# Kernel optimization log

Measured on AMD Instinct MI355X. Metric: run time of the kernel, lower is better.

The kernel has to match this reference:

```python
import jax, jax.numpy as jnp
import numpy as np

L = 16            # number of levels
F = 2             # features per level
T = 1 << 17       # hashmap size per level (power of 2)
N_TREES = 8       # forest blocks
N = 2_000_000     # query points
RES = np.array([16, 22, 30, 41, 55, 75, 102, 139, 188, 256, 348, 472, 642, 872, 1184, 1608], dtype=np.int64)
# 8 trilinear corner offsets [8,3]
OFFS = np.stack(np.meshgrid([0, 1], [0, 1], [0, 1], indexing='ij'), axis=-1).reshape(8, 3).astype(np.int32)
PRIMES = (np.uint32(1), np.uint32(2654435761), np.uint32(805459861))


def _hash(coords):
    # coords: [N,8,3] int32 grid corner coords -> [N,8] table index (NGP spatial hash)
    c = coords.astype(jnp.uint32)
    h = (c[..., 0] * PRIMES[0]) ^ (c[..., 1] * PRIMES[1]) ^ (c[..., 2] * PRIMES[2])
    return (h & jnp.uint32(T - 1)).astype(jnp.int32)


def setup_inputs() -> dict:
    key = jax.random.key(0)
    k1, k2, k3 = jax.random.split(key, 3)
    block_x = jax.random.uniform(k1, (N, 3), minval=-1.0, maxval=1.0, dtype=jnp.float32)
    bound = 1e-4
    params = jax.random.uniform(k2, (N_TREES, L, T, F), minval=-bound, maxval=bound, dtype=jnp.float32)
    block_inds = jax.random.randint(k3, (N,), 0, N_TREES)
    return {"block_x": block_x, "params": params, "block_inds": block_inds}


def reference(block_x, params, block_inds):
    # block_x in [-1,1]^3 -> [0,1]^3 (matches `block_x / 2.0 + 0.5` in forward)
    x01 = block_x * 0.5 + 0.5
    offs = jnp.asarray(OFFS)                    # [8,3]
    offs_b = jnp.asarray(OFFS, dtype=bool)      # [8,3]
    outs = []
    for l in range(L):
        R = int(RES[l])
        pos = x01 * (R - 1)                     # [N,3]
        p0 = jnp.floor(pos)
        w = pos - p0                            # trilinear fracs [N,3]
        p0i = p0.astype(jnp.int32)
        corners = jnp.clip(p0i[:, None, :] + offs[None], 0, R - 1)   # [N,8,3]
        idx = _hash(corners)                                          # [N,8]
        feats = params[block_inds[:, None], l, idx, :]                # [N,8,F] per-tree gather
        wc = jnp.prod(jnp.where(offs_b[None], w[:, None, :], 1.0 - w[:, None, :]), axis=-1)  # [N,8]
        outs.append(jnp.einsum('nc,ncf->nf', wc, feats))              # [N,F]
    return jnp.concatenate(outs, axis=-1)        # [N, L*F]
```

## Files before the change

kernel.cpp:

```cpp
#include <hip/hip_runtime.h>

#define NLEVELS 16
#define TSIZE 131072
#define TMASK (TSIZE - 1)
#define NBUCK 32768

typedef float f32x4 __attribute__((ext_vector_type(4)));

__device__ __constant__ float RM1_TAB[16] = {
    15.f, 21.f, 29.f, 40.f, 54.f, 74.f, 101.f, 138.f,
    187.f, 255.f, 347.f, 471.f, 641.f, 871.f, 1183.f, 1607.f
};

__device__ __forceinline__ unsigned spread4(unsigned v) {
    v = (v | (v << 4)) & 0x0C3u;
    v = (v | (v << 2)) & 0x249u;
    return v;
}

__device__ __forceinline__ unsigned bucket_key(float x, float y, float z, unsigned tree) {
    const int cx = min(max((int)((x * 0.5f + 0.5f) * 16.f), 0), 15);
    const int cy = min(max((int)((y * 0.5f + 0.5f) * 16.f), 0), 15);
    const int cz = min(max((int)((z * 0.5f + 0.5f) * 16.f), 0), 15);
    const unsigned m = spread4((unsigned)cx) | (spread4((unsigned)cy) << 1)
                     | (spread4((unsigned)cz) << 2);
    return (tree << 12) | m;
}


__global__ __launch_bounds__(256) void k_hist(const float* __restrict__ xs,
                                              const int* __restrict__ inds, int N,
                                              unsigned* __restrict__ hist) {
    const int i = blockIdx.x * 256 + threadIdx.x;
    if (i >= N) return;
    const unsigned key = bucket_key(xs[3 * i], xs[3 * i + 1], xs[3 * i + 2],
                                    (unsigned)(inds[i] & 7));
    atomicAdd(&hist[key], 1u);
}

__global__ __launch_bounds__(1024) void k_scan(const unsigned* __restrict__ hist,
                                               unsigned* __restrict__ cursor) {
    __shared__ unsigned sums[1024];
    const int t = threadIdx.x;
    const int per = NBUCK / 1024;
    unsigned s = 0;
    #pragma unroll
    for (int j = 0; j < per; ++j) s += hist[t * per + j];
    sums[t] = s;
    __syncthreads();
    for (int off = 1; off < 1024; off <<= 1) {
        const unsigned add = (t >= off) ? sums[t - off] : 0u;
        __syncthreads();
        sums[t] += add;
        __syncthreads();
    }
    unsigned run = (t == 0) ? 0u : sums[t - 1];
    #pragma unroll
    for (int j = 0; j < per; ++j) {
        cursor[t * per + j] = run;
        run += hist[t * per + j];
    }
}

__global__ __launch_bounds__(256) void k_scatter(const float* __restrict__ xs,
                                                 const int* __restrict__ inds, int N,
                                                 unsigned* __restrict__ cursor,
                                                 float4* __restrict__ sorted) {
    const int i = blockIdx.x * 256 + threadIdx.x;
    if (i >= N) return;
    const float x = xs[3 * i], y = xs[3 * i + 1], z = xs[3 * i + 2];
    const unsigned tree = (unsigned)(inds[i] & 7);
    const unsigned key = bucket_key(x, y, z, tree);
    const unsigned pos = atomicAdd(&cursor[key], 1u);
    sorted[pos] = make_float4(x, y, z, __uint_as_float(((unsigned)i) | (tree << 24)));
}


__global__ __launch_bounds__(256) void k_main(const float4* __restrict__ sorted,
                                              const float* __restrict__ params,
                                              float4* __restrict__ ws2,
                                              float4* __restrict__ out4,
                                              int N, int nc, int direct) {
    const int b = blockIdx.x;
    const int k = b & 7;
    const int chunk = b >> 3;
    const int i = chunk * 256 + threadIdx.x;
    if (i >= N) return;

    const float4 p = sorted[i];
    const unsigned wbits = __float_as_uint(p.w);
    const int n = (int)(wbits & 0xFFFFFFu);
    const int tree = (int)(wbits >> 24);

    float acc[4];

    #pragma unroll
    for (int kk = 0; kk < 2; ++kk) {
        const int l = 2 * k + kk;
        const float rm1 = RM1_TAB[l];
        const int rmax = (int)rm1;

        const float px = (p.x * 0.5f + 0.5f) * rm1;
        const float py = (p.y * 0.5f + 0.5f) * rm1;
        const float pz = (p.z * 0.5f + 0.5f) * rm1;
        const float fx = floorf(px), fy = floorf(py), fz = floorf(pz);
        const float wx = px - fx, wy = py - fy, wz = pz - fz;
        const int ix = (int)fx, iy = (int)fy, iz = (int)fz;

        const int x0 = min(max(ix, 0), rmax), x1 = min(max(ix + 1, 0), rmax);
        const int y0 = min(max(iy, 0), rmax), y1 = min(max(iy + 1, 0), rmax);
        const int z0 = min(max(iz, 0), rmax), z1 = min(max(iz + 1, 0), rmax);

        const unsigned hx0 = (unsigned)x0;
        const unsigned hx1 = (unsigned)x1;
        const unsigned hy0 = (unsigned)y0 * 2654435761u;
        const unsigned hy1 = (unsigned)y1 * 2654435761u;
        const unsigned hz0 = (unsigned)z0 * 805459861u;
        const unsigned hz1 = (unsigned)z1 * 805459861u;

        const float2* __restrict__ tbl =
            (const float2*)(params + (size_t)(tree * NLEVELS + l) * (TSIZE * 2));

        const unsigned m00 = hy0 ^ hz0;
        const unsigned m01 = hy0 ^ hz1;
        const unsigned m10 = hy1 ^ hz0;
        const unsigned m11 = hy1 ^ hz1;
        const unsigned i000 = (hx0 ^ m00) & TMASK;
        const unsigned i001 = (hx0 ^ m01) & TMASK;
        const unsigned i010 = (hx0 ^ m10) & TMASK;
        const unsigned i011 = (hx0 ^ m11) & TMASK;

        float2 f000, f001, f010, f011, f100, f101, f110, f111;

        const bool pairOK = ((x0 & 1) == 0) && (x1 == x0 + 1);
        if (pairOK) {
            const float4* __restrict__ tbl4 = (const float4*)tbl;
            const float4 q00 = tbl4[i000 >> 1];
            const float4 q01 = tbl4[i001 >> 1];
            const float4 q10 = tbl4[i010 >> 1];
            const float4 q11 = tbl4[i011 >> 1];
            f000 = (i000 & 1) ? make_float2(q00.z, q00.w) : make_float2(q00.x, q00.y);
            f100 = (i000 & 1) ? make_float2(q00.x, q00.y) : make_float2(q00.z, q00.w);
            f001 = (i001 & 1) ? make_float2(q01.z, q01.w) : make_float2(q01.x, q01.y);
            f101 = (i001 & 1) ? make_float2(q01.x, q01.y) : make_float2(q01.z, q01.w);
            f010 = (i010 & 1) ? make_float2(q10.z, q10.w) : make_float2(q10.x, q10.y);
            f110 = (i010 & 1) ? make_float2(q10.x, q10.y) : make_float2(q10.z, q10.w);
            f011 = (i011 & 1) ? make_float2(q11.z, q11.w) : make_float2(q11.x, q11.y);
            f111 = (i011 & 1) ? make_float2(q11.x, q11.y) : make_float2(q11.z, q11.w);
        } else {
            const unsigned i100 = (hx1 ^ m00) & TMASK;
            const unsigned i101 = (hx1 ^ m01) & TMASK;
            const unsigned i110 = (hx1 ^ m10) & TMASK;
            const unsigned i111 = (hx1 ^ m11) & TMASK;
            f000 = tbl[i000]; f001 = tbl[i001];
            f010 = tbl[i010]; f011 = tbl[i011];
            f100 = tbl[i100]; f101 = tbl[i101];
            f110 = tbl[i110]; f111 = tbl[i111];
        }

        const float wx0 = 1.f - wx, wy0 = 1.f - wy, wz0 = 1.f - wz;

        const float w000 = wx0 * wy0 * wz0;
        const float w001 = wx0 * wy0 * wz;
        const float w010 = wx0 * wy  * wz0;
        const float w011 = wx0 * wy  * wz;
        const float w100 = wx  * wy0 * wz0;
        const float w101 = wx  * wy0 * wz;
        const float w110 = wx  * wy  * wz0;
        const float w111 = wx  * wy  * wz;

        float a0 = 0.f, a1 = 0.f;
        a0 = fmaf(w000, f000.x, a0); a1 = fmaf(w000, f000.y, a1);
        a0 = fmaf(w001, f001.x, a0); a1 = fmaf(w001, f001.y, a1);
        a0 = fmaf(w010, f010.x, a0); a1 = fmaf(w010, f010.y, a1);
        a0 = fmaf(w011, f011.x, a0); a1 = fmaf(w011, f011.y, a1);
        a0 = fmaf(w100, f100.x, a0); a1 = fmaf(w100, f100.y, a1);
        a0 = fmaf(w101, f101.x, a0); a1 = fmaf(w101, f101.y, a1);
        a0 = fmaf(w110, f110.x, a0); a1 = fmaf(w110, f110.y, a1);
        a0 = fmaf(w111, f111.x, a0); a1 = fmaf(w111, f111.y, a1);

        acc[2 * kk + 0] = a0;
        acc[2 * kk + 1] = a1;
    }

    const float4 v = make_float4(acc[0], acc[1], acc[2], acc[3]);
    if (direct) {
        out4[(size_t)n * 8 + k] = v;
    } else {
        const size_t stride = (size_t)nc * 256;
        __builtin_nontemporal_store(*(const f32x4*)&v,
                                    (f32x4*)&ws2[(size_t)k * stride + i]);
    }
}


__global__ __launch_bounds__(256) void k_final(const float4* __restrict__ sorted,
                                               const float4* __restrict__ ws2,
                                               float4* __restrict__ out4,
                                               int N, int nc) {
    const int i = blockIdx.x * 256 + threadIdx.x;
    if (i >= N) return;
    const unsigned wbits = __float_as_uint(sorted[i].w);
    const int n = (int)(wbits & 0xFFFFFFu);
    const size_t stride = (size_t)nc * 256;
    #pragma unroll
    for (int k = 0; k < 8; ++k) {
        f32x4 v = __builtin_nontemporal_load((const f32x4*)&ws2[(size_t)k * stride + i]);
        out4[(size_t)n * 8 + k] = *(const float4*)&v;
    }
}


__global__ __launch_bounds__(256) void lotd_fwd_fused(
    const float* __restrict__ xs, const float* __restrict__ params,
    const int* __restrict__ inds, float* __restrict__ out, int N)
{
    const int g = blockIdx.x * 256 + threadIdx.x;
    const int n = g >> 4;
    if (n >= N) return;
    const int l = g & 15;
    const float rm1 = RM1_TAB[l];
    const int rmax = (int)rm1;
    const float x = xs[3 * n], y = xs[3 * n + 1], z = xs[3 * n + 2];
    const int tree = inds[n];
    const float px = (x * 0.5f + 0.5f) * rm1;
    const float py = (y * 0.5f + 0.5f) * rm1;
    const float pz = (z * 0.5f + 0.5f) * rm1;
    const float fx = floorf(px), fy = floorf(py), fz = floorf(pz);
    const float wx = px - fx, wy = py - fy, wz = pz - fz;
    const int ix = (int)fx, iy = (int)fy, iz = (int)fz;
    const int x0 = min(max(ix, 0), rmax), x1 = min(max(ix + 1, 0), rmax);
    const int y0 = min(max(iy, 0), rmax), y1 = min(max(iy + 1, 0), rmax);
    const int z0 = min(max(iz, 0), rmax), z1 = min(max(iz + 1, 0), rmax);
    const unsigned hx0 = (unsigned)x0, hx1 = (unsigned)x1;
    const unsigned hy0 = (unsigned)y0 * 2654435761u, hy1 = (unsigned)y1 * 2654435761u;
    const unsigned hz0 = (unsigned)z0 * 805459861u,  hz1 = (unsigned)z1 * 805459861u;
    const float2* tbl = (const float2*)(params + (size_t)(tree * NLEVELS + l) * (TSIZE * 2));
    const float2 f000 = tbl[(hx0 ^ hy0 ^ hz0) & TMASK];
    const float2 f001 = tbl[(hx0 ^ hy0 ^ hz1) & TMASK];
    const float2 f010 = tbl[(hx0 ^ hy1 ^ hz0) & TMASK];
    const float2 f011 = tbl[(hx0 ^ hy1 ^ hz1) & TMASK];
    const float2 f100 = tbl[(hx1 ^ hy0 ^ hz0) & TMASK];
    const float2 f101 = tbl[(hx1 ^ hy0 ^ hz1) & TMASK];
    const float2 f110 = tbl[(hx1 ^ hy1 ^ hz0) & TMASK];
    const float2 f111 = tbl[(hx1 ^ hy1 ^ hz1) & TMASK];
    const float wx0 = 1.f - wx, wy0 = 1.f - wy, wz0 = 1.f - wz;
    float a0 = 0.f, a1 = 0.f;
    a0 = fmaf(wx0*wy0*wz0, f000.x, a0); a1 = fmaf(wx0*wy0*wz0, f000.y, a1);
    a0 = fmaf(wx0*wy0*wz , f001.x, a0); a1 = fmaf(wx0*wy0*wz , f001.y, a1);
    a0 = fmaf(wx0*wy *wz0, f010.x, a0); a1 = fmaf(wx0*wy *wz0, f010.y, a1);
    a0 = fmaf(wx0*wy *wz , f011.x, a0); a1 = fmaf(wx0*wy *wz , f011.y, a1);
    a0 = fmaf(wx *wy0*wz0, f100.x, a0); a1 = fmaf(wx *wy0*wz0, f100.y, a1);
    a0 = fmaf(wx *wy0*wz , f101.x, a0); a1 = fmaf(wx *wy0*wz , f101.y, a1);
    a0 = fmaf(wx *wy *wz0, f110.x, a0); a1 = fmaf(wx *wy *wz0, f110.y, a1);
    a0 = fmaf(wx *wy *wz , f111.x, a0); a1 = fmaf(wx *wy *wz , f111.y, a1);
    ((float2*)out)[(size_t)n * 16 + l] = make_float2(a0, a1);
}

extern "C" void kernel_launch(void* const* d_in, const int* in_sizes, int n_in,
                              void* d_out, int out_size, void* d_ws, size_t ws_size,
                              hipStream_t stream) {
    const float* xs     = (const float*)d_in[0];
    const float* params = (const float*)d_in[1];
    const int*   inds   = (const int*)d_in[2];
    float*       out    = (float*)d_out;

    const int N = in_sizes[0] / 3;
    const int nc = (N + 255) / 256;

    const size_t hist_bytes   = (size_t)NBUCK * 4;
    const size_t head_bytes   = 2 * hist_bytes;
    const size_t sorted_bytes = ((size_t)N * 16 + 255) & ~(size_t)255;
    const size_t ws2_bytes    = (size_t)nc * 256 * 8 * 16;
    const size_t need_B = head_bytes + sorted_bytes;
    const size_t need_A = need_B + ws2_bytes;

    if (ws_size < need_B) {
        const int total = N * NLEVELS;
        lotd_fwd_fused<<<(total + 255) / 256, 256, 0, stream>>>(xs, params, inds, out, N);
        return;
    }

    unsigned* hist   = (unsigned*)d_ws;
    unsigned* cursor = (unsigned*)((char*)d_ws + hist_bytes);
    float4*   sorted = (float4*)((char*)d_ws + head_bytes);
    float4*   ws2    = (float4*)((char*)d_ws + head_bytes + sorted_bytes);

    hipMemsetAsync(hist, 0, hist_bytes, stream);
    k_hist<<<nc, 256, 0, stream>>>(xs, inds, N, hist);
    k_scan<<<1, 1024, 0, stream>>>(hist, cursor);
    k_scatter<<<nc, 256, 0, stream>>>(xs, inds, N, cursor, sorted);

    const int direct = (ws_size < need_A) ? 1 : 0;
    k_main<<<nc * 8, 256, 0, stream>>>(sorted, params,
                                       direct ? nullptr : ws2,
                                       (float4*)out, N, nc, direct);
    if (!direct)
        k_final<<<nc, 256, 0, stream>>>(sorted, ws2, (float4*)out, N, nc);
}
```

Before: 949.5 us.

## Drop staging buffer, write outputs directly with banded level rotation

Removes the intermediate ws2 buffer and the k_final gather kernel, so k_main now scatters its float4 results straight to the output rows. The level pair each block handles is rotated by band index, so concurrently running blocks touch different level tables and spread the gather traffic. It also issues both levels' table loads before either FMA reduction to raise memory-level parallelism. The trade-off is uncoalesced scattered writes in place of a coalesced staging pass, in exchange for saving a full write-plus-read of the intermediate data and one launch.

```diff
diff --git a/kernel.cpp b/kernel.cpp
--- a/kernel.cpp
+++ b/kernel.cpp
@@ -76,14 +76,103 @@
 }
 
 
+__device__ __forceinline__ void level_load(const float4 p, int tree, int l,
+                                           const float* __restrict__ params,
+                                           float2 f[8],
+                                           float& wx, float& wy, float& wz) {
+    const float rm1 = RM1_TAB[l];
+    const int rmax = (int)rm1;
+
+    const float px = (p.x * 0.5f + 0.5f) * rm1;
+    const float py = (p.y * 0.5f + 0.5f) * rm1;
+    const float pz = (p.z * 0.5f + 0.5f) * rm1;
+    const float fx = floorf(px), fy = floorf(py), fz = floorf(pz);
+    wx = px - fx; wy = py - fy; wz = pz - fz;
+    const int ix = (int)fx, iy = (int)fy, iz = (int)fz;
+
+    const int x0 = min(max(ix, 0), rmax), x1 = min(max(ix + 1, 0), rmax);
+    const int y0 = min(max(iy, 0), rmax), y1 = min(max(iy + 1, 0), rmax);
+    const int z0 = min(max(iz, 0), rmax), z1 = min(max(iz + 1, 0), rmax);
+
+    const unsigned hx0 = (unsigned)x0;
+    const unsigned hx1 = (unsigned)x1;
+    const unsigned hy0 = (unsigned)y0 * 2654435761u;
+    const unsigned hy1 = (unsigned)y1 * 2654435761u;
+    const unsigned hz0 = (unsigned)z0 * 805459861u;
+    const unsigned hz1 = (unsigned)z1 * 805459861u;
+
+    const float2* __restrict__ tbl =
+        (const float2*)(params + (size_t)(tree * NLEVELS + l) * (TSIZE * 2));
+
+    const unsigned m00 = hy0 ^ hz0;
+    const unsigned m01 = hy0 ^ hz1;
+    const unsigned m10 = hy1 ^ hz0;
+    const unsigned m11 = hy1 ^ hz1;
+    const unsigned i000 = (hx0 ^ m00) & TMASK;
+    const unsigned i001 = (hx0 ^ m01) & TMASK;
+    const unsigned i010 = (hx0 ^ m10) & TMASK;
+    const unsigned i011 = (hx0 ^ m11) & TMASK;
+
+    const bool pairOK = ((x0 & 1) == 0) && (x1 == x0 + 1);
+    if (pairOK) {
+        const float4* __restrict__ tbl4 = (const float4*)tbl;
+        const float4 q00 = tbl4[i000 >> 1];
+        const float4 q01 = tbl4[i001 >> 1];
+        const float4 q10 = tbl4[i010 >> 1];
+        const float4 q11 = tbl4[i011 >> 1];
+        f[0] = (i000 & 1) ? make_float2(q00.z, q00.w) : make_float2(q00.x, q00.y);
+        f[4] = (i000 & 1) ? make_float2(q00.x, q00.y) : make_float2(q00.z, q00.w);
+        f[1] = (i001 & 1) ? make_float2(q01.z, q01.w) : make_float2(q01.x, q01.y);
+        f[5] = (i001 & 1) ? make_float2(q01.x, q01.y) : make_float2(q01.z, q01.w);
+        f[2] = (i010 & 1) ? make_float2(q10.z, q10.w) : make_float2(q10.x, q10.y);
+        f[6] = (i010 & 1) ? make_float2(q10.x, q10.y) : make_float2(q10.z, q10.w);
+        f[3] = (i011 & 1) ? make_float2(q11.z, q11.w) : make_float2(q11.x, q11.y);
+        f[7] = (i011 & 1) ? make_float2(q11.x, q11.y) : make_float2(q11.z, q11.w);
+    } else {
+        const unsigned i100 = (hx1 ^ m00) & TMASK;
+        const unsigned i101 = (hx1 ^ m01) & TMASK;
+        const unsigned i110 = (hx1 ^ m10) & TMASK;
+        const unsigned i111 = (hx1 ^ m11) & TMASK;
+        f[0] = tbl[i000]; f[1] = tbl[i001];
+        f[2] = tbl[i010]; f[3] = tbl[i011];
+        f[4] = tbl[i100]; f[5] = tbl[i101];
+        f[6] = tbl[i110]; f[7] = tbl[i111];
+    }
+}
+
+__device__ __forceinline__ float2 level_fma(const float2 f[8],
+                                            float wx, float wy, float wz) {
+    const float wx0 = 1.f - wx, wy0 = 1.f - wy, wz0 = 1.f - wz;
+    const float w0 = wx0 * wy0 * wz0;
+    const float w1 = wx0 * wy0 * wz;
+    const float w2 = wx0 * wy  * wz0;
+    const float w3 = wx0 * wy  * wz;
+    const float w4 = wx  * wy0 * wz0;
+    const float w5 = wx  * wy0 * wz;
+    const float w6 = wx  * wy  * wz0;
+    const float w7 = wx  * wy  * wz;
+    float a0 = 0.f, a1 = 0.f;
+    a0 = fmaf(w0, f[0].x, a0); a1 = fmaf(w0, f[0].y, a1);
+    a0 = fmaf(w1, f[1].x, a0); a1 = fmaf(w1, f[1].y, a1);
+    a0 = fmaf(w2, f[2].x, a0); a1 = fmaf(w2, f[2].y, a1);
+    a0 = fmaf(w3, f[3].x, a0); a1 = fmaf(w3, f[3].y, a1);
+    a0 = fmaf(w4, f[4].x, a0); a1 = fmaf(w4, f[4].y, a1);
+    a0 = fmaf(w5, f[5].x, a0); a1 = fmaf(w5, f[5].y, a1);
+    a0 = fmaf(w6, f[6].x, a0); a1 = fmaf(w6, f[6].y, a1);
+    a0 = fmaf(w7, f[7].x, a0); a1 = fmaf(w7, f[7].y, a1);
+    return make_float2(a0, a1);
+}
+
+
 __global__ __launch_bounds__(256) void k_main(const float4* __restrict__ sorted,
                                               const float* __restrict__ params,
-                                              float4* __restrict__ ws2,
                                               float4* __restrict__ out4,
-                                              int N, int nc, int direct) {
+                                              int N, int nc, int band_sz) {
     const int b = blockIdx.x;
-    const int k = b & 7;
+    const int j = b & 7;
     const int chunk = b >> 3;
+    const int band = chunk / band_sz;
+    const int v = (j + band) & 7;
     const int i = chunk * 256 + threadIdx.x;
     if (i >= N) return;
 
@@ -92,122 +181,16 @@
     const int n = (int)(wbits & 0xFFFFFFu);
     const int tree = (int)(wbits >> 24);
 
-    float acc[4];
-
-    #pragma unroll
-    for (int kk = 0; kk < 2; ++kk) {
-        const int l = 2 * k + kk;
-        const float rm1 = RM1_TAB[l];
-        const int rmax = (int)rm1;
-
-        const float px = (p.x * 0.5f + 0.5f) * rm1;
-        const float py = (p.y * 0.5f + 0.5f) * rm1;
-        const float pz = (p.z * 0.5f + 0.5f) * rm1;
-        const float fx = floorf(px), fy = floorf(py), fz = floorf(pz);
-        const float wx = px - fx, wy = py - fy, wz = pz - fz;
-        const int ix = (int)fx, iy = (int)fy, iz = (int)fz;
-
-        const int x0 = min(max(ix, 0), rmax), x1 = min(max(ix + 1, 0), rmax);
-        const int y0 = min(max(iy, 0), rmax), y1 = min(max(iy + 1, 0), rmax);
-        const int z0 = min(max(iz, 0), rmax), z1 = min(max(iz + 1, 0), rmax);
-
-        const unsigned hx0 = (unsigned)x0;
-        const unsigned hx1 = (unsigned)x1;
-        const unsigned hy0 = (unsigned)y0 * 2654435761u;
-        const unsigned hy1 = (unsigned)y1 * 2654435761u;
-        const unsigned hz0 = (unsigned)z0 * 805459861u;
-        const unsigned hz1 = (unsigned)z1 * 805459861u;
-
-        const float2* __restrict__ tbl =
-            (const float2*)(params + (size_t)(tree * NLEVELS + l) * (TSIZE * 2));
-
-        const unsigned m00 = hy0 ^ hz0;
-        const unsigned m01 = hy0 ^ hz1;
-        const unsigned m10 = hy1 ^ hz0;
-        const unsigned m11 = hy1 ^ hz1;
-        const unsigned i000 = (hx0 ^ m00) & TMASK;
-        const unsigned i001 = (hx0 ^ m01) & TMASK;
-        const unsigned i010 = (hx0 ^ m10) & TMASK;
-        const unsigned i011 = (hx0 ^ m11) & TMASK;
-
-        float2 f000, f001, f010, f011, f100, f101, f110, f111;
-
-        const bool pairOK = ((x0 & 1) == 0) && (x1 == x0 + 1);
-        if (pairOK) {
-            const float4* __restrict__ tbl4 = (const float4*)tbl;
-            const float4 q00 = tbl4[i000 >> 1];
-            const float4 q01 = tbl4[i001 >> 1];
-            const float4 q10 = tbl4[i010 >> 1];
-            const float4 q11 = tbl4[i011 >> 1];
-            f000 = (i000 & 1) ? make_float2(q00.z, q00.w) : make_float2(q00.x, q00.y);
-            f100 = (i000 & 1) ? make_float2(q00.x, q00.y) : make_float2(q00.z, q00.w);
-            f001 = (i001 & 1) ? make_float2(q01.z, q01.w) : make_float2(q01.x, q01.y);
-            f101 = (i001 & 1) ? make_float2(q01.x, q01.y) : make_float2(q01.z, q01.w);
-            f010 = (i010 & 1) ? make_float2(q10.z, q10.w) : make_float2(q10.x, q10.y);
-            f110 = (i010 & 1) ? make_float2(q10.x, q10.y) : make_float2(q10.z, q10.w);
-            f011 = (i011 & 1) ? make_float2(q11.z, q11.w) : make_float2(q11.x, q11.y);
-            f111 = (i011 & 1) ? make_float2(q11.x, q11.y) : make_float2(q11.z, q11.w);
-        } else {
-            const unsigned i100 = (hx1 ^ m00) & TMASK;
-            const unsigned i101 = (hx1 ^ m01) & TMASK;
-            const unsigned i110 = (hx1 ^ m10) & TMASK;
-            const unsigned i111 = (hx1 ^ m11) & TMASK;
-            f000 = tbl[i000]; f001 = tbl[i001];
-            f010 = tbl[i010]; f011 = tbl[i011];
-            f100 = tbl[i100]; f101 = tbl[i101];
-            f110 = tbl[i110]; f111 = tbl[i111];
-        }
-
-        const float wx0 = 1.f - wx, wy0 = 1.f - wy, wz0 = 1.f - wz;
-
-        const float w000 = wx0 * wy0 * wz0;
-        const float w001 = wx0 * wy0 * wz;
-        const float w010 = wx0 * wy  * wz0;
-        const float w011 = wx0 * wy  * wz;
-        const float w100 = wx  * wy0 * wz0;
-        const float w101 = wx  * wy0 * wz;
-        const float w110 = wx  * wy  * wz0;
-        const float w111 = wx  * wy  * wz;
-
-        float a0 = 0.f, a1 = 0.f;
-        a0 = fmaf(w000, f000.x, a0); a1 = fmaf(w000, f000.y, a1);
-        a0 = fmaf(w001, f001.x, a0); a1 = fmaf(w001, f001.y, a1);
-        a0 = fmaf(w010, f010.x, a0); a1 = fmaf(w010, f010.y, a1);
-        a0 = fmaf(w011, f011.x, a0); a1 = fmaf(w011, f011.y, a1);
-        a0 = fmaf(w100, f100.x, a0); a1 = fmaf(w100, f100.y, a1);
-        a0 = fmaf(w101, f101.x, a0); a1 = fmaf(w101, f101.y, a1);
-        a0 = fmaf(w110, f110.x, a0); a1 = fmaf(w110, f110.y, a1);
-        a0 = fmaf(w111, f111.x, a0); a1 = fmaf(w111, f111.y, a1);
-
-        acc[2 * kk + 0] = a0;
-        acc[2 * kk + 1] = a1;
-    }
-
-    const float4 v = make_float4(acc[0], acc[1], acc[2], acc[3]);
-    if (direct) {
-        out4[(size_t)n * 8 + k] = v;
-    } else {
-        const size_t stride = (size_t)nc * 256;
-        __builtin_nontemporal_store(*(const f32x4*)&v,
-                                    (f32x4*)&ws2[(size_t)k * stride + i]);
-    }
-}
-
-
-__global__ __launch_bounds__(256) void k_final(const float4* __restrict__ sorted,
-                                               const float4* __restrict__ ws2,
-                                               float4* __restrict__ out4,
-                                               int N, int nc) {
-    const int i = blockIdx.x * 256 + threadIdx.x;
-    if (i >= N) return;
-    const unsigned wbits = __float_as_uint(sorted[i].w);
-    const int n = (int)(wbits & 0xFFFFFFu);
-    const size_t stride = (size_t)nc * 256;
-    #pragma unroll
-    for (int k = 0; k < 8; ++k) {
-        f32x4 v = __builtin_nontemporal_load((const f32x4*)&ws2[(size_t)k * stride + i]);
-        out4[(size_t)n * 8 + k] = *(const float4*)&v;
-    }
+    float2 fA[8], fB[8];
+    float wxA, wyA, wzA, wxB, wyB, wzB;
+
+    level_load(p, tree, 2 * v,     params, fA, wxA, wyA, wzA);
+    level_load(p, tree, 2 * v + 1, params, fB, wxB, wyB, wzB);
+
+    const float2 rA = level_fma(fA, wxA, wyA, wzA);
+    const float2 rB = level_fma(fB, wxB, wyB, wzB);
+
+    out4[(size_t)n * 8 + v] = make_float4(rA.x, rA.y, rB.x, rB.y);
 }
 
 
@@ -267,15 +250,14 @@
 
     const int N = in_sizes[0] / 3;
     const int nc = (N + 255) / 256;
+    const int band_sz = (nc + 7) / 8;
 
     const size_t hist_bytes   = (size_t)NBUCK * 4;
     const size_t head_bytes   = 2 * hist_bytes;
     const size_t sorted_bytes = ((size_t)N * 16 + 255) & ~(size_t)255;
-    const size_t ws2_bytes    = (size_t)nc * 256 * 8 * 16;
-    const size_t need_B = head_bytes + sorted_bytes;
-    const size_t need_A = need_B + ws2_bytes;
-
-    if (ws_size < need_B) {
+    const size_t need = head_bytes + sorted_bytes;
+
+    if (ws_size < need) {
         const int total = N * NLEVELS;
         lotd_fwd_fused<<<(total + 255) / 256, 256, 0, stream>>>(xs, params, inds, out, N);
         return;
@@ -284,17 +266,11 @@
     unsigned* hist   = (unsigned*)d_ws;
     unsigned* cursor = (unsigned*)((char*)d_ws + hist_bytes);
     float4*   sorted = (float4*)((char*)d_ws + head_bytes);
-    float4*   ws2    = (float4*)((char*)d_ws + head_bytes + sorted_bytes);
 
     hipMemsetAsync(hist, 0, hist_bytes, stream);
     k_hist<<<nc, 256, 0, stream>>>(xs, inds, N, hist);
     k_scan<<<1, 1024, 0, stream>>>(hist, cursor);
     k_scatter<<<nc, 256, 0, stream>>>(xs, inds, N, cursor, sorted);
 
-    const int direct = (ws_size < need_A) ? 1 : 0;
-    k_main<<<nc * 8, 256, 0, stream>>>(sorted, params,
-                                       direct ? nullptr : ws2,
-                                       (float4*)out, N, nc, direct);
-    if (!direct)
-        k_final<<<nc, 256, 0, stream>>>(sorted, ws2, (float4*)out, N, nc);
-}
+    k_main<<<nc * 8, 256, 0, stream>>>(sorted, params, (float4*)out, N, nc, band_sz);
+}
```

New measurement: 854.9 us. 1.11x faster.
